# Kernel optimization log

Measured on AMD Instinct MI355X. Metric: run time of the kernel, lower is better.

## Reference

```python
import jax, jax.numpy as jnp
import numpy as np

B, N, A, M, H, KD, VD, O = 256, 2048, 256, 256, 8, 32, 32, 256
EPS = 1e-10

def setup_inputs() -> dict:
    key = jax.random.key(0)
    ks = jax.random.split(key, 8)
    return {
        "q_data": jax.random.normal(ks[0], (B, N, A), dtype=jnp.float32),
        "m_data": jax.random.normal(ks[1], (B, N, M), dtype=jnp.float32),
        "q_mask": jnp.ones((B, N, 1), dtype=jnp.float32),
        "bias": jnp.zeros((B, 1, N), dtype=jnp.float32),
        "query_w": 0.02 * jax.random.normal(ks[2], (A, H, KD), dtype=jnp.float32),
        "key_w": 0.02 * jax.random.normal(ks[3], (M, KD), dtype=jnp.float32),
        "value_w": 0.02 * jax.random.normal(ks[4], (M, VD), dtype=jnp.float32),
        "gating_w": 0.02 * jax.random.normal(ks[5], (A, H, VD), dtype=jnp.float32),
        "gating_b": jnp.zeros((H, VD), dtype=jnp.float32),
        "output_w": 0.02 * jax.random.normal(ks[6], (H, VD, O), dtype=jnp.float32),
        "output_b": jnp.zeros((O,), dtype=jnp.float32),
    }

def reference(q_data, m_data, q_mask, bias, query_w, key_w, value_w,
              gating_w, gating_b, output_w, output_b):
    # masked mean over the query axis: q_mask [B,N,1] broadcasts over channels
    q_avg = jnp.sum(q_mask * q_data, axis=1) / (jnp.sum(q_mask, axis=1) + EPS)  # [B,A]
    kd = query_w.shape[-1]
    q = jnp.einsum('ba,ahc->bhc', q_avg, query_w) * kd ** (-0.5)  # [B,H,KD]
    k = jnp.einsum('bka,ac->bkc', m_data, key_w)                  # [B,N,KD]
    v = jnp.einsum('bka,ac->bkc', m_data, value_w)                # [B,N,VD]
    # the incoming `bias` arg is overwritten by the module, as in the original
    attn_bias = 1e9 * (q_mask[:, None, :, 0] - 1.0)               # [B,1,N]
    logits = jnp.einsum('bhc,bkc->bhk', q, k) + attn_bias         # [B,H,N]
    weights = jax.nn.softmax(logits, axis=-1)
    weighted_avg = jnp.einsum('bhk,bkc->bhc', weights, v)         # [B,H,VD]
    # gating == True
    gate = jax.nn.sigmoid(jnp.einsum('bqc,chv->bqhv', q_data, gating_w) + gating_b)
    gated = weighted_avg[:, None] * gate                          # [B,N,H,VD]
    out = jnp.einsum('bqhc,hco->bqo', gated, output_w) + output_b # [B,N,O]
    return out
```

## Files before the change

### kernel.cpp

```cpp
#include <hip/hip_runtime.h>

#define B_ 256
#define N_ 2048
#define A_ 256
#define M_ 256
#define H_ 8
#define KD_ 32
#define VD_ 32
#define O_ 256

typedef float f32x4 __attribute__((ext_vector_type(4)));
typedef __bf16 bf16x8 __attribute__((ext_vector_type(8)));
typedef unsigned short u16x8 __attribute__((ext_vector_type(8)));

union FragU { u16x8 u; bf16x8 b; };

__device__ __forceinline__ unsigned short f2bf(float f) {
  union { __bf16 b; unsigned short u; } c;
  c.b = (__bf16)f;
  return c.u;
}
__device__ __forceinline__ float bf2f(unsigned short h) {
  return __uint_as_float(((unsigned int)h) << 16);
}

__device__ __forceinline__ void gll16(const void* gsrc, void* ldst) {
  __builtin_amdgcn_global_load_lds(
      (const __attribute__((address_space(1))) void*)gsrc,
      (__attribute__((address_space(3))) void*)ldst, 16, 0, 0);
}

__global__ void pack_weights(const float* __restrict__ gating_w,
                             const float* __restrict__ output_w,
                             const float* __restrict__ key_w,
                             const float* __restrict__ value_w,
                             unsigned short* __restrict__ wg,
                             unsigned short* __restrict__ wo,
                             unsigned short* __restrict__ wkv) {
  int idx = blockIdx.x * 256 + threadIdx.x;
  int j = idx & 7;
  int lane = (idx >> 3) & 63;
  int rest = idx >> 9;
  int kc = rest & 7, ct = rest >> 3;
  int row = kc * 32 + ((lane >> 4) << 3) + j;
  int col = ct * 16 + (lane & 15);
  wg[idx] = f2bf(gating_w[row * 256 + col]);
  wo[idx] = f2bf(output_w[row * 256 + col]);
  if (idx < 16384) {
    float v = (col < 32) ? key_w[row * 32 + col] : value_w[row * 32 + (col - 32)];
    wkv[idx] = f2bf(v);
  }
}

__global__ void reduce_q(const float* __restrict__ qd, const float* __restrict__ qm,
                         const float* __restrict__ qw, float* __restrict__ q_out) {
  int b = blockIdx.x;
  int t = threadIdx.x;
  int l = t & 63, g = t >> 6;
  const float* qdb = qd + (size_t)b * N_ * A_;
  const float* qmb = qm + (size_t)b * N_;
  f32x4 sum = {0.f, 0.f, 0.f, 0.f};
  float msum = 0.f;
  for (int n = g; n < N_; n += 16) {
    float m = qmb[n];
    msum += m;
    f32x4 v = *(const f32x4*)(qdb + (size_t)n * A_ + l * 4);
    sum += m * v;
  }
  __shared__ float s[16][256];
  __shared__ float ms[16];
  __shared__ float qavg[256];
  *(f32x4*)&s[g][l * 4] = sum;
  if (l == 0) ms[g] = msum;
  __syncthreads();
  if (t < 256) {
    float tot = 0.f;
#pragma unroll
    for (int k = 0; k < 16; k++) tot += s[k][t];
    float mt = 0.f;
#pragma unroll
    for (int k = 0; k < 16; k++) mt += ms[k];
    qavg[t] = tot / (mt + 1e-10f);
  }
  __syncthreads();
  if (t < 256) {
    float acc = 0.f;
    for (int a2 = 0; a2 < 256; a2++) acc += qavg[a2] * qw[a2 * 256 + t];
    q_out[b * 256 + t] = acc * 0.17677669529663687f;
  }
}

__global__ void kv_gemm(const float* __restrict__ md,
                        const unsigned short* __restrict__ wkv,
                        unsigned short* __restrict__ k_ws,
                        unsigned short* __restrict__ v_ws) {
  int t = threadIdx.x;
  int w = t >> 6, l = t & 63, q = l >> 4, l15 = l & 15;
  size_t r0 = (size_t)blockIdx.x * 128;
  int b = (int)(r0 >> 11);
  int n0 = (int)(r0 & 2047);
  f32x4 acc[2][4] = {};
  for (int kc = 0; kc < 8; kc++) {
    FragU bfr[4];
#pragma unroll
    for (int ct = 0; ct < 4; ct++)
      bfr[ct].u = *(const u16x8*)(wkv + (((ct * 8 + kc) * 64 + l) << 3));
    FragU af[2];
#pragma unroll
    for (int rt = 0; rt < 2; rt++) {
      size_t row = r0 + (size_t)(w * 32 + rt * 16 + l15);
      const float4* s4 = (const float4*)(md + row * 256 + kc * 32 + q * 8);
      float4 u0 = s4[0], u1 = s4[1];
      af[rt].u = (u16x8){f2bf(u0.x), f2bf(u0.y), f2bf(u0.z), f2bf(u0.w),
                         f2bf(u1.x), f2bf(u1.y), f2bf(u1.z), f2bf(u1.w)};
    }
#pragma unroll
    for (int ct = 0; ct < 4; ct++) {
      acc[0][ct] = __builtin_amdgcn_mfma_f32_16x16x32_bf16(af[0].b, bfr[ct].b, acc[0][ct], 0, 0, 0);
      acc[1][ct] = __builtin_amdgcn_mfma_f32_16x16x32_bf16(af[1].b, bfr[ct].b, acc[1][ct], 0, 0, 0);
    }
  }
#pragma unroll
  for (int rt = 0; rt < 2; rt++)
#pragma unroll
    for (int ct = 0; ct < 4; ct++)
#pragma unroll
      for (int r = 0; r < 4; r++) {
        int rloc = w * 32 + rt * 16 + q * 4 + r;
        if (ct < 2) {
          k_ws[(r0 + rloc) * 32 + ct * 16 + l15] = f2bf(acc[rt][ct][r]);
        } else {
          v_ws[((size_t)b * 32 + (ct - 2) * 16 + l15) * N_ + (n0 + rloc)] = f2bf(acc[rt][ct][r]);
        }
      }
}

__global__ void attn_softmax(const unsigned short* __restrict__ k_ws,
                             const unsigned short* __restrict__ v_ws,
                             const float* __restrict__ qv,
                             const float* __restrict__ qm,
                             float* __restrict__ wa) {
  int b = blockIdx.x, t = threadIdx.x;
  __shared__ float lg[8][2048];
  __shared__ float red[4][256];
  __shared__ float inv_s[8];
  const float* qb = qv + b * 256;
  const float* qmb = qm + (size_t)b * N_;
  for (int n = t; n < N_; n += 1024) {
    const u16x8* kr = (const u16x8*)(k_ws + ((size_t)(b * N_ + n)) * 32);
    float kf[32];
#pragma unroll
    for (int c8 = 0; c8 < 2; c8++) {
      u16x8 kk = kr[c8];
#pragma unroll
      for (int j = 0; j < 8; j++) kf[c8 * 8 + j] = bf2f(kk[j]);
    }
    u16x8 kk2 = kr[0];
    (void)kk2;
#pragma unroll
    for (int c8 = 2; c8 < 4; c8++) {
      u16x8 kk = kr[c8 - 2 + 2];
      (void)kk;
    }
    {
      u16x8 ka = kr[0], kb2 = kr[1], kc2 = kr[2], kd2 = kr[3];
#pragma unroll
      for (int j = 0; j < 8; j++) {
        kf[j]      = bf2f(ka[j]);
        kf[8 + j]  = bf2f(kb2[j]);
        kf[16 + j] = bf2f(kc2[j]);
        kf[24 + j] = bf2f(kd2[j]);
      }
    }
    float bias_n = 1e9f * (qmb[n] - 1.0f);
#pragma unroll
    for (int h = 0; h < 8; h++) {
      float d = 0.f;
#pragma unroll
      for (int c = 0; c < 32; c++) d += qb[h * 32 + c] * kf[c];
      lg[h][n] = d + bias_n;
    }
  }
  __syncthreads();
  if (t < 256) {
    int h = t >> 5, i = t & 31;
    float m = -3.0e38f;
    for (int n = i; n < N_; n += 32) m = fmaxf(m, lg[h][n]);
#pragma unroll
    for (int off = 16; off; off >>= 1) m = fmaxf(m, __shfl_xor(m, off));
    float s = 0.f;
    for (int n = i; n < N_; n += 32) {
      float e = __expf(lg[h][n] - m);
      lg[h][n] = e;
      s += e;
    }
#pragma unroll
    for (int off = 16; off; off >>= 1) s += __shfl_xor(s, off);
    if (i == 0) inv_s[h] = 1.0f / s;
  }
  __syncthreads();
  {
    int c = t & 31, h = (t >> 5) & 7, nq = t >> 8;
    const u16x8* vb = (const u16x8*)(v_ws + ((size_t)b * 32 + c) * N_ + nq * 512);
    const f32x4* lg4 = (const f32x4*)&lg[h][nq * 512];
    float acc = 0.f;
#pragma unroll 4
    for (int n8 = 0; n8 < 64; n8++) {
      u16x8 vv = vb[n8];
      f32x4 p0 = lg4[n8 * 2], p1 = lg4[n8 * 2 + 1];
      acc += p0[0] * bf2f(vv[0]);
      acc += p0[1] * bf2f(vv[1]);
      acc += p0[2] * bf2f(vv[2]);
      acc += p0[3] * bf2f(vv[3]);
      acc += p1[0] * bf2f(vv[4]);
      acc += p1[1] * bf2f(vv[5]);
      acc += p1[2] * bf2f(vv[6]);
      acc += p1[3] * bf2f(vv[7]);
    }
    red[nq][t & 255] = acc;
  }
  __syncthreads();
  if (t < 256) {
    float r = red[0][t] + red[1][t] + red[2][t] + red[3][t];
    wa[b * 256 + t] = r * inv_s[t >> 5];
  }
}

__launch_bounds__(256, 3)
__global__ void gate_out(const float* __restrict__ qd,
                         const unsigned short* __restrict__ wg,
                         const unsigned short* __restrict__ wo,
                         const float* __restrict__ wa,
                         const float* __restrict__ gb,
                         const float* __restrict__ ob,
                         float* __restrict__ out) {
  int blk = blockIdx.x;
  int b = blk >> 5, tile = blk & 31;
  int t = threadIdx.x;
  int w = t >> 6, l = t & 63, q = l >> 4, l15 = l & 15;
  __shared__ __attribute__((aligned(16))) unsigned short wsg[2][8192];
  __shared__ __attribute__((aligned(16))) unsigned short Pt[2][4][16][40];
  __shared__ float wa_s[256], gb_s[256], ob_s[256];
  wa_s[t] = wa[b * 256 + t];
  gb_s[t] = gb[t];
  ob_s[t] = ob[t];
  size_t rowbase = (size_t)b * N_ + tile * 64;

  {
    const char* wgb = (const char*)wg;
#pragma unroll
    for (int i = 0; i < 4; i++) {
      int ch = i * 4 + w;
      gll16(wgb + ch * 1024 + l * 16, (char*)&wsg[0][0] + ch * 1024);
    }
  }

  FragU af[8];
  {
    const float* src = qd + (rowbase + (size_t)(w * 16 + l15)) * 256 + q * 8;
#pragma unroll
    for (int kc = 0; kc < 8; kc++) {
      float4 u0 = *(const float4*)(src + kc * 32);
      float4 u1 = *(const float4*)(src + kc * 32 + 4);
      af[kc].u = (u16x8){f2bf(u0.x), f2bf(u0.y), f2bf(u0.z), f2bf(u0.w),
                         f2bf(u1.x), f2bf(u1.y), f2bf(u1.z), f2bf(u1.w)};
    }
  }
  f32x4 acc[4][4] = {};
  __syncthreads();

  for (int g = 0; g < 8; g++) {
    int cur = g & 1;
    if (g < 7) {
      const char* wgb = (const char*)wg + (size_t)(g + 1) * 16384;
#pragma unroll
      for (int i = 0; i < 4; i++) {
        int ch = i * 4 + w;
        gll16(wgb + ch * 1024 + l * 16, (char*)&wsg[cur ^ 1][0] + ch * 1024);
      }
    }
    f32x4 gacc[2] = {};
#pragma unroll
    for (int kc = 0; kc < 8; kc++) {
      FragU b0, b1;
      b0.u = *(const u16x8*)(&wsg[cur][0] + (kc * 64 + l) * 8);
      b1.u = *(const u16x8*)(&wsg[cur][0] + ((8 + kc) * 64 + l) * 8);
      gacc[0] = __builtin_amdgcn_mfma_f32_16x16x32_bf16(af[kc].b, b0.b, gacc[0], 0, 0, 0);
      gacc[1] = __builtin_amdgcn_mfma_f32_16x16x32_bf16(af[kc].b, b1.b, gacc[1], 0, 0, 0);
    }
#pragma unroll
    for (int ctl = 0; ctl < 2; ctl++) {
      int colg = ctl * 16 + l15;
      int col = g * 32 + colg;
      float wav = wa_s[col], gbv = gb_s[col];
#pragma unroll
      for (int r = 0; r < 4; r++) {
        float x = gacc[ctl][r] + gbv;
        float gate = 1.0f / (1.0f + __expf(-x));
        Pt[cur][w][q * 4 + r][colg] = f2bf(wav * gate);
      }
    }

    __syncthreads();

    FragU pf[4];
#pragma unroll
    for (int rt = 0; rt < 4; rt++)
      pf[rt].u = *(const u16x8*)&Pt[cur][rt][l15][q * 8];
#pragma unroll
    for (int ct2 = 0; ct2 < 4; ct2++) {
      FragU bo;
      bo.u = *(const u16x8*)((const char*)wo + (size_t)(w * 4 + ct2) * 8192 +
                             (size_t)g * 1024 + l * 16);
#pragma unroll
      for (int rt = 0; rt < 4; rt++)
        acc[rt][ct2] = __builtin_amdgcn_mfma_f32_16x16x32_bf16(pf[rt].b, bo.b, acc[rt][ct2], 0, 0, 0);
    }
  }
#pragma unroll
  for (int rt = 0; rt < 4; rt++) {
#pragma unroll
    for (int ct2 = 0; ct2 < 4; ct2++) {
      int col = w * 64 + ct2 * 16 + l15;
      float obv = ob_s[col];
      size_t orow = (rowbase + (size_t)(rt * 16 + q * 4)) * 256 + col;
#pragma unroll
      for (int r = 0; r < 4; r++)
        out[orow + (size_t)r * 256] = acc[rt][ct2][r] + obv;
    }
  }
}

extern "C" void kernel_launch(void* const* d_in, const int* in_sizes, int n_in,
                              void* d_out, int out_size, void* d_ws, size_t ws_size,
                              hipStream_t stream) {
  const float* q_data   = (const float*)d_in[0];
  const float* m_data   = (const float*)d_in[1];
  const float* q_mask   = (const float*)d_in[2];
  const float* query_w  = (const float*)d_in[4];
  const float* key_w    = (const float*)d_in[5];
  const float* value_w  = (const float*)d_in[6];
  const float* gating_w = (const float*)d_in[7];
  const float* gating_b = (const float*)d_in[8];
  const float* output_w = (const float*)d_in[9];
  const float* output_b = (const float*)d_in[10];
  float* out = (float*)d_out;

  char* ws = (char*)d_ws;
  float* q_ws            = (float*)(ws);
  float* wa_ws           = (float*)(ws + (256 << 10));
  unsigned short* wg_ws  = (unsigned short*)(ws + (512 << 10));
  unsigned short* wo_ws  = (unsigned short*)(ws + (640 << 10));
  unsigned short* wkv_ws = (unsigned short*)(ws + (768 << 10));
  unsigned short* k_wsp  = (unsigned short*)(ws + (800 << 10));
  unsigned short* v_wsp  = (unsigned short*)(ws + (800 << 10) + ((size_t)32 << 20));

  pack_weights<<<256, 256, 0, stream>>>(gating_w, output_w, key_w, value_w,
                                        wg_ws, wo_ws, wkv_ws);
  reduce_q<<<B_, 1024, 0, stream>>>(q_data, q_mask, query_w, q_ws);
  kv_gemm<<<(B_ * N_) / 128, 256, 0, stream>>>(m_data, wkv_ws, k_wsp, v_wsp);
  attn_softmax<<<B_, 1024, 0, stream>>>(k_wsp, v_wsp, q_ws, q_mask, wa_ws);
  gate_out<<<(B_ * N_) / 64, 256, 0, stream>>>(q_data, wg_ws, wo_ws, wa_ws,
                                               gating_b, output_b, out);
}
```

Before: 1.474 ms.

## Enlarge gate_out row tile to 128 and stage output weights in LDS

gate_out now processes 128 rows per block, and each wave owns 32 rows across all 256 output columns instead of 64 columns across shared rows. Output-weight slices are staged in shared memory alongside the gating weights, and the double buffer is replaced with single buffers guarded by two barriers per step. This halves the number of blocks and the redundant weight traffic per row, at the cost of more accumulator registers (occupancy hint lowered to 2) and less load/compute overlap. The attn_softmax key-load code also drops its dead redundant loads.

```diff
diff --git a/kernel.cpp b/kernel.cpp
--- a/kernel.cpp
+++ b/kernel.cpp
@@ -148,29 +148,14 @@
   const float* qmb = qm + (size_t)b * N_;
   for (int n = t; n < N_; n += 1024) {
     const u16x8* kr = (const u16x8*)(k_ws + ((size_t)(b * N_ + n)) * 32);
+    u16x8 ka = kr[0], kb2 = kr[1], kc2 = kr[2], kd2 = kr[3];
     float kf[32];
 #pragma unroll
-    for (int c8 = 0; c8 < 2; c8++) {
-      u16x8 kk = kr[c8];
-#pragma unroll
-      for (int j = 0; j < 8; j++) kf[c8 * 8 + j] = bf2f(kk[j]);
-    }
-    u16x8 kk2 = kr[0];
-    (void)kk2;
-#pragma unroll
-    for (int c8 = 2; c8 < 4; c8++) {
-      u16x8 kk = kr[c8 - 2 + 2];
-      (void)kk;
-    }
-    {
-      u16x8 ka = kr[0], kb2 = kr[1], kc2 = kr[2], kd2 = kr[3];
-#pragma unroll
-      for (int j = 0; j < 8; j++) {
-        kf[j]      = bf2f(ka[j]);
-        kf[8 + j]  = bf2f(kb2[j]);
-        kf[16 + j] = bf2f(kc2[j]);
-        kf[24 + j] = bf2f(kd2[j]);
-      }
+    for (int j = 0; j < 8; j++) {
+      kf[j]      = bf2f(ka[j]);
+      kf[8 + j]  = bf2f(kb2[j]);
+      kf[16 + j] = bf2f(kc2[j]);
+      kf[24 + j] = bf2f(kd2[j]);
     }
     float bias_n = 1e9f * (qmb[n] - 1.0f);
 #pragma unroll
@@ -226,7 +211,7 @@
   }
 }
 
-__launch_bounds__(256, 3)
+__launch_bounds__(256, 2)
 __global__ void gate_out(const float* __restrict__ qd,
                          const unsigned short* __restrict__ wg,
                          const unsigned short* __restrict__ wo,
@@ -235,100 +220,112 @@
                          const float* __restrict__ ob,
                          float* __restrict__ out) {
   int blk = blockIdx.x;
-  int b = blk >> 5, tile = blk & 31;
+  int b = blk >> 4, tile = blk & 15;
   int t = threadIdx.x;
   int w = t >> 6, l = t & 63, q = l >> 4, l15 = l & 15;
-  __shared__ __attribute__((aligned(16))) unsigned short wsg[2][8192];
-  __shared__ __attribute__((aligned(16))) unsigned short Pt[2][4][16][40];
+  __shared__ __attribute__((aligned(16))) unsigned short wsg[8192];
+  __shared__ __attribute__((aligned(16))) unsigned short wso[8192];
+  __shared__ __attribute__((aligned(16))) unsigned short Pt[4][2][16][40];
   __shared__ float wa_s[256], gb_s[256], ob_s[256];
   wa_s[t] = wa[b * 256 + t];
   gb_s[t] = gb[t];
   ob_s[t] = ob[t];
-  size_t rowbase = (size_t)b * N_ + tile * 64;
+  size_t rowbase = (size_t)b * N_ + tile * 128;
 
   {
     const char* wgb = (const char*)wg;
+    const char* wob = (const char*)wo;
 #pragma unroll
     for (int i = 0; i < 4; i++) {
       int ch = i * 4 + w;
-      gll16(wgb + ch * 1024 + l * 16, (char*)&wsg[0][0] + ch * 1024);
-    }
-  }
-
-  FragU af[8];
-  {
-    const float* src = qd + (rowbase + (size_t)(w * 16 + l15)) * 256 + q * 8;
+      gll16(wgb + ch * 1024 + l * 16, (char*)wsg + ch * 1024);
+      gll16(wob + ch * 8192 + l * 16, (char*)wso + ch * 1024);
+    }
+  }
+
+  FragU af[2][8];
+#pragma unroll
+  for (int rt = 0; rt < 2; rt++) {
+    const float* src = qd + (rowbase + (size_t)(w * 32 + rt * 16 + l15)) * 256 + q * 8;
 #pragma unroll
     for (int kc = 0; kc < 8; kc++) {
       float4 u0 = *(const float4*)(src + kc * 32);
       float4 u1 = *(const float4*)(src + kc * 32 + 4);
-      af[kc].u = (u16x8){f2bf(u0.x), f2bf(u0.y), f2bf(u0.z), f2bf(u0.w),
-                         f2bf(u1.x), f2bf(u1.y), f2bf(u1.z), f2bf(u1.w)};
-    }
-  }
-  f32x4 acc[4][4] = {};
+      af[rt][kc].u = (u16x8){f2bf(u0.x), f2bf(u0.y), f2bf(u0.z), f2bf(u0.w),
+                             f2bf(u1.x), f2bf(u1.y), f2bf(u1.z), f2bf(u1.w)};
+    }
+  }
+  f32x4 acc[2][16] = {};
   __syncthreads();
 
   for (int g = 0; g < 8; g++) {
-    int cur = g & 1;
+    f32x4 gacc[2][2] = {};
+#pragma unroll
+    for (int kc = 0; kc < 8; kc++) {
+      FragU b0, b1;
+      b0.u = *(const u16x8*)(wsg + (kc * 64 + l) * 8);
+      b1.u = *(const u16x8*)(wsg + ((8 + kc) * 64 + l) * 8);
+      gacc[0][0] = __builtin_amdgcn_mfma_f32_16x16x32_bf16(af[0][kc].b, b0.b, gacc[0][0], 0, 0, 0);
+      gacc[0][1] = __builtin_amdgcn_mfma_f32_16x16x32_bf16(af[0][kc].b, b1.b, gacc[0][1], 0, 0, 0);
+      gacc[1][0] = __builtin_amdgcn_mfma_f32_16x16x32_bf16(af[1][kc].b, b0.b, gacc[1][0], 0, 0, 0);
+      gacc[1][1] = __builtin_amdgcn_mfma_f32_16x16x32_bf16(af[1][kc].b, b1.b, gacc[1][1], 0, 0, 0);
+    }
+#pragma unroll
+    for (int rt = 0; rt < 2; rt++)
+#pragma unroll
+      for (int ctl = 0; ctl < 2; ctl++) {
+        int colg = ctl * 16 + l15;
+        int col = g * 32 + colg;
+        float wav = wa_s[col], gbv = gb_s[col];
+#pragma unroll
+        for (int r = 0; r < 4; r++) {
+          float x = gacc[rt][ctl][r] + gbv;
+          float gate = 1.0f / (1.0f + __expf(-x));
+          Pt[w][rt][q * 4 + r][colg] = f2bf(wav * gate);
+        }
+      }
+    FragU pf[2];
+#pragma unroll
+    for (int rt = 0; rt < 2; rt++)
+      pf[rt].u = *(const u16x8*)&Pt[w][rt][l15][q * 8];
+
+    __syncthreads();
     if (g < 7) {
       const char* wgb = (const char*)wg + (size_t)(g + 1) * 16384;
 #pragma unroll
       for (int i = 0; i < 4; i++) {
         int ch = i * 4 + w;
-        gll16(wgb + ch * 1024 + l * 16, (char*)&wsg[cur ^ 1][0] + ch * 1024);
+        gll16(wgb + ch * 1024 + l * 16, (char*)wsg + ch * 1024);
       }
     }
-    f32x4 gacc[2] = {};
-#pragma unroll
-    for (int kc = 0; kc < 8; kc++) {
-      FragU b0, b1;
-      b0.u = *(const u16x8*)(&wsg[cur][0] + (kc * 64 + l) * 8);
-      b1.u = *(const u16x8*)(&wsg[cur][0] + ((8 + kc) * 64 + l) * 8);
-      gacc[0] = __builtin_amdgcn_mfma_f32_16x16x32_bf16(af[kc].b, b0.b, gacc[0], 0, 0, 0);
-      gacc[1] = __builtin_amdgcn_mfma_f32_16x16x32_bf16(af[kc].b, b1.b, gacc[1], 0, 0, 0);
-    }
-#pragma unroll
-    for (int ctl = 0; ctl < 2; ctl++) {
-      int colg = ctl * 16 + l15;
-      int col = g * 32 + colg;
-      float wav = wa_s[col], gbv = gb_s[col];
-#pragma unroll
-      for (int r = 0; r < 4; r++) {
-        float x = gacc[ctl][r] + gbv;
-        float gate = 1.0f / (1.0f + __expf(-x));
-        Pt[cur][w][q * 4 + r][colg] = f2bf(wav * gate);
+#pragma unroll
+    for (int ct = 0; ct < 16; ct++) {
+      FragU bo;
+      bo.u = *(const u16x8*)(wso + (ct * 64 + l) * 8);
+      acc[0][ct] = __builtin_amdgcn_mfma_f32_16x16x32_bf16(pf[0].b, bo.b, acc[0][ct], 0, 0, 0);
+      acc[1][ct] = __builtin_amdgcn_mfma_f32_16x16x32_bf16(pf[1].b, bo.b, acc[1][ct], 0, 0, 0);
+    }
+    __syncthreads();
+    if (g < 7) {
+      const char* wob = (const char*)wo + (size_t)(g + 1) * 1024;
+#pragma unroll
+      for (int i = 0; i < 4; i++) {
+        int ch = i * 4 + w;
+        gll16(wob + ch * 8192 + l * 16, (char*)wso + ch * 1024);
       }
     }
-
-    __syncthreads();
-
-    FragU pf[4];
-#pragma unroll
-    for (int rt = 0; rt < 4; rt++)
-      pf[rt].u = *(const u16x8*)&Pt[cur][rt][l15][q * 8];
-#pragma unroll
-    for (int ct2 = 0; ct2 < 4; ct2++) {
-      FragU bo;
-      bo.u = *(const u16x8*)((const char*)wo + (size_t)(w * 4 + ct2) * 8192 +
-                             (size_t)g * 1024 + l * 16);
-#pragma unroll
-      for (int rt = 0; rt < 4; rt++)
-        acc[rt][ct2] = __builtin_amdgcn_mfma_f32_16x16x32_bf16(pf[rt].b, bo.b, acc[rt][ct2], 0, 0, 0);
-    }
-  }
-#pragma unroll
-  for (int rt = 0; rt < 4; rt++) {
-#pragma unroll
-    for (int ct2 = 0; ct2 < 4; ct2++) {
-      int col = w * 64 + ct2 * 16 + l15;
+  }
+#pragma unroll
+  for (int rt = 0; rt < 2; rt++)
+#pragma unroll
+    for (int ct = 0; ct < 16; ct++) {
+      int col = ct * 16 + l15;
       float obv = ob_s[col];
-      size_t orow = (rowbase + (size_t)(rt * 16 + q * 4)) * 256 + col;
+      size_t orow = (rowbase + (size_t)(w * 32 + rt * 16 + q * 4)) * 256 + col;
 #pragma unroll
       for (int r = 0; r < 4; r++)
-        out[orow + (size_t)r * 256] = acc[rt][ct2][r] + obv;
-    }
-  }
+        out[orow + (size_t)r * 256] = acc[rt][ct][r] + obv;
+    }
 }
 
 extern "C" void kernel_launch(void* const* d_in, const int* in_sizes, int n_in,
@@ -360,6 +357,6 @@
   reduce_q<<<B_, 1024, 0, stream>>>(q_data, q_mask, query_w, q_ws);
   kv_gemm<<<(B_ * N_) / 128, 256, 0, stream>>>(m_data, wkv_ws, k_wsp, v_wsp);
   attn_softmax<<<B_, 1024, 0, stream>>>(k_wsp, v_wsp, q_ws, q_mask, wa_ws);
-  gate_out<<<(B_ * N_) / 64, 256, 0, stream>>>(q_data, wg_ws, wo_ws, wa_ws,
-                                               gating_b, output_b, out);
-}
+  gate_out<<<(B_ * N_) / 128, 256, 0, stream>>>(q_data, wg_ws, wo_ws, wa_ws,
+                                                gating_b, output_b, out);
+}
```

Result: no change. 1.458 ms (-1.1%).
